# Kernel tuning notes

Measured on AMD Instinct MI355X. Metric: run time of the kernel, lower is better.

The kernel has to match this reference:

```python
import jax, jax.numpy as jnp
import numpy as np
from jax import lax

B, CIN, COUT, K = 4, 128, 128, 3
Z = X = Y = 32
EPS = 1e-8


def setup_inputs() -> dict:
    key = jax.random.key(0)
    k1, k2, k3 = jax.random.split(key, 3)
    x = jax.random.normal(k1, (B, CIN, Z, X, Y), dtype=jnp.float32)
    S = jax.random.normal(k2, (B, CIN), dtype=jnp.float32)
    weight = jax.random.normal(k3, (COUT, CIN, K, K, K), dtype=jnp.float32)
    return {"x": x, "S": S, "weight": weight}


def reference(x, S, weight):
    b, cin, z, xx, yy = x.shape
    cout = weight.shape[0]
    # Per-sample modulated weight: [B, cout, cin, k, k, k]
    W = weight[None] * (S[:, None, :, None, None, None] + 1.0)
    # Demodulation: L2-normalize each (b, cout) filter
    d = lax.rsqrt(jnp.sum(W * W, axis=(2, 3, 4, 5), keepdims=True) + EPS)
    W = W * d
    # Grouped conv3d with groups=B (stride=1, dilation=1 -> same padding = (k-1)//2)
    pad = (K - 1) // 2
    xr = x.reshape(1, b * cin, z, xx, yy)
    Wr = W.reshape(b * cout, cin, K, K, K)
    out = lax.conv_general_dilated(
        xr, Wr,
        window_strides=(1, 1, 1),
        padding=[(pad, pad)] * 3,
        feature_group_count=b,
        dimension_numbers=("NCDHW", "OIDHW", "NCDHW"),
    )
    return out.reshape(b, cout, z, xx, yy)
```

## Files before the change

kernel.cpp:

```cpp
#include <hip/hip_runtime.h>

#define B_    4
#define CIN_  128
#define COUT_ 128
#define EPSF  1e-8f

typedef short  short8  __attribute__((ext_vector_type(8)));
typedef unsigned short ushort8 __attribute__((ext_vector_type(8)));
typedef float  f32x16  __attribute__((ext_vector_type(16)));

__device__ __forceinline__ unsigned short f2bf(float f) {
    union { float f; unsigned int u; } v; v.f = f;
    unsigned int r = (v.u + 0x7fffu + ((v.u >> 16) & 1u)) >> 16;
    return (unsigned short)r;
}

__global__ __launch_bounds__(128) void scale_kernel(const float* __restrict__ S,
                                                    const float* __restrict__ w,
                                                    float* __restrict__ d) {
    const int co = blockIdx.x;
    const int ci = threadIdx.x;
    const float* wp = w + ((size_t)co * CIN_ + ci) * 27;
    float wsq = 0.f;
#pragma unroll
    for (int k = 0; k < 27; ++k) { float v = wp[k]; wsq += v * v; }
    __shared__ float red[128];
    for (int b = 0; b < B_; ++b) {
        float s = S[b * CIN_ + ci] + 1.0f;
        red[ci] = s * s * wsq;
        __syncthreads();
        for (int off = 64; off > 0; off >>= 1) {
            if (ci < off) red[ci] += red[ci + off];
            __syncthreads();
        }
        if (ci == 0) d[b * COUT_ + co] = rsqrtf(red[0] + EPSF);
        __syncthreads();
    }
}

__global__ __launch_bounds__(256) void wt_kernel(const float* __restrict__ w,
                                                 unsigned short* __restrict__ wtf) {
    int idx = blockIdx.x * 256 + threadIdx.x;
    int e  = idx & 7;
    int l  = (idx >> 3) & 63;
    int c  = (idx >> 9) & 7;
    int ct = (idx >> 12) & 3;
    int ko = idx >> 14;
    int co = ct * 32 + (l & 31);
    int ci = c * 16 + (l >> 5) * 8 + e;
    wtf[idx] = f2bf(w[((size_t)co * CIN_ + ci) * 27 + ko]);
}

__global__ __launch_bounds__(256) void xt_kernel(const float* __restrict__ x,
                                                 const float* __restrict__ S,
                                                 unsigned short* __restrict__ xT) {
    __shared__ float ls[128 * 33];
    const int xx = blockIdx.x, z = blockIdx.y, b = blockIdx.z;
    const int tid = threadIdx.x;
    const size_t base = (size_t)b * 4194304 + (size_t)z * 1024 + xx * 32;
#pragma unroll
    for (int it = 0; it < 4; ++it) {
        int i = tid + it * 256;
        int ci = i >> 3, y4 = (i & 7) * 4;
        float4 v = *(const float4*)(x + base + (size_t)ci * 32768 + y4);
        float s = S[b * CIN_ + ci] + 1.0f;
        ls[ci * 33 + y4 + 0] = v.x * s;
        ls[ci * 33 + y4 + 1] = v.y * s;
        ls[ci * 33 + y4 + 2] = v.z * s;
        ls[ci * 33 + y4 + 3] = v.w * s;
    }
    __syncthreads();
    const size_t obase = (size_t)((b * 32 + z) * 32 + xx) * 4096;
#pragma unroll
    for (int it = 0; it < 2; ++it) {
        int i = tid + it * 256;
        int y = i >> 4, c = (i >> 1) & 7, h = i & 1;
        ushort8 v;
#pragma unroll
        for (int j = 0; j < 8; ++j) v[j] = f2bf(ls[(c * 16 + h * 8 + j) * 33 + y]);
        *(ushort8*)(xT + obase + c * 512 + y * 16 + h * 8) = v;
    }
}

__global__ __launch_bounds__(256, 2) void conv_mfma(const unsigned short* __restrict__ xT,
                                                    const unsigned short* __restrict__ wtf,
                                                    const float* __restrict__ dscale,
                                                    float* __restrict__ out) {
    __shared__ char smem[2][26112];
    const int tid  = threadIdx.x;
    const int lane = tid & 63;
    const int wv   = tid >> 6;
    const int z0 = (blockIdx.x >> 4) * 4;
    const int x0 = (blockIdx.x & 15) * 2;
    const int b  = blockIdx.y;

    int goff[7];
    const int lbase = tid * 16;
#pragma unroll
    for (int s = 0; s < 7; ++s) {
        int g = tid + s * 256;
        goff[s] = -2;
        if (g < 1632) {
            int row = g / 68, rem = g - row * 68;
            int h = rem / 34, yi = rem - h * 34;
            int zg = z0 + (row >> 2) - 1;
            int xg = x0 + (row & 3) - 1;
            goff[s] = -1;
            if ((unsigned)zg < 32u && (unsigned)xg < 32u && yi >= 1 && yi <= 32)
                goff[s] = ((b * 32 + zg) * 32 + xg) * 8192 + (yi - 1) * 32 + h * 16;
        }
    }

    const char* xTb = (const char*)xT;
    const char* wtb = (const char*)wtf;
    const int bperlane = ((lane >> 5) * 34 + (lane & 31)) * 16;
    const int aperlane = lane * 16;

    f32x16 acc[4][2];
#pragma unroll
    for (int cz = 0; cz < 4; ++cz)
#pragma unroll
        for (int cx = 0; cx < 2; ++cx)
#pragma unroll
            for (int r = 0; r < 16; ++r) acc[cz][cx][r] = 0.f;

    ushort8 st[7];
#pragma unroll
    for (int s = 0; s < 7; ++s) {
        ushort8 v = {0, 0, 0, 0, 0, 0, 0, 0};
        if (goff[s] >= 0) v = *(const ushort8*)(xTb + goff[s]);
        st[s] = v;
    }
#pragma unroll
    for (int s = 0; s < 7; ++s)
        if (goff[s] != -2) *(ushort8*)(&smem[0][0] + lbase + s * 4096) = st[s];
    __syncthreads();

    for (int c = 0; c < 8; ++c) {
        if (c < 7) {
#pragma unroll
            for (int s = 0; s < 7; ++s) {
                ushort8 v = {0, 0, 0, 0, 0, 0, 0, 0};
                if (goff[s] >= 0) v = *(const ushort8*)(xTb + goff[s] + (c + 1) * 1024);
                st[s] = v;
            }
        }
        const char* buf   = smem[c & 1];
        const char* abase = wtb + c * 1024 + wv * 8192;
#pragma unroll
        for (int ky = 0; ky < 3; ++ky) {
            short8 a[9];
#pragma unroll
            for (int t = 0; t < 9; ++t)
                a[t] = *(const short8*)(abase + (t * 3 + ky) * 32768 + aperlane);
#pragma unroll
            for (int zr = 0; zr < 6; ++zr) {
                short8 bf[4];
#pragma unroll
                for (int xr = 0; xr < 4; ++xr)
                    bf[xr] = *(const short8*)(buf + ((zr * 4 + xr) * 68 + ky) * 16 + bperlane);
#pragma unroll
                for (int cz = 0; cz < 4; ++cz) {
                    const int kz = zr - cz;
                    if (kz >= 0 && kz <= 2) {
#pragma unroll
                        for (int cx = 0; cx < 2; ++cx)
#pragma unroll
                        for (int kx = 0; kx < 3; ++kx)
                            acc[cz][cx] = __builtin_amdgcn_mfma_f32_32x32x16_bf16(
                                a[kz * 3 + kx], bf[cx + kx], acc[cz][cx], 0, 0, 0);
                    }
                }
            }
        }
        if (c < 7) {
            char* nbuf = smem[(c + 1) & 1];
#pragma unroll
            for (int s = 0; s < 7; ++s)
                if (goff[s] != -2) *(ushort8*)(nbuf + lbase + s * 4096) = st[s];
        }
        __syncthreads();
    }

    float dd[16];
#pragma unroll
    for (int r = 0; r < 16; ++r)
        dd[r] = dscale[b * COUT_ + wv * 32 + (r & 3) + 8 * (r >> 2) + 4 * (lane >> 5)];
#pragma unroll
    for (int cz = 0; cz < 4; ++cz)
#pragma unroll
    for (int cx = 0; cx < 2; ++cx) {
        size_t ob = (((size_t)(b * COUT_ + wv * 32) * 32 + (z0 + cz)) * 32 + (x0 + cx)) * 32 + (lane & 31);
#pragma unroll
        for (int r = 0; r < 16; ++r) {
            int row = (r & 3) + 8 * (r >> 2) + 4 * (lane >> 5);
            out[ob + (size_t)row * 32768] = acc[cz][cx][r] * dd[r];
        }
    }
}

__global__ __launch_bounds__(256, 4) void conv_kernel(const float* __restrict__ x,
                                                      const float* __restrict__ S,
                                                      const float* __restrict__ w,
                                                      const float* __restrict__ dscale,
                                                      float* __restrict__ out) {
    __shared__ float xs[6][6][36];
    __shared__ float wsm[27][16];
    const int tid = threadIdx.x;
    const int zt  = blockIdx.x >> 3;
    const int xt  = blockIdx.x & 7;
    const int co0 = blockIdx.y * 16;
    const int b   = blockIdx.z;
    const int z0 = zt * 4, x0 = xt * 4;
    const int lane = tid & 63;
    const int cg = tid >> 6;
    const int zz = (lane >> 4) & 3;
    const int xx = (lane >> 2) & 3;
    const int y0 = (lane & 3) * 8;
    float acc[4][8];
#pragma unroll
    for (int c = 0; c < 4; ++c)
#pragma unroll
        for (int j = 0; j < 8; ++j) acc[c][j] = 0.f;
    for (int ci = 0; ci < CIN_; ++ci) {
        __syncthreads();
        const float* xb = x + (size_t)(b * CIN_ + ci) * 32768;
        const float smod = S[b * CIN_ + ci] + 1.0f;
#pragma unroll
        for (int t = 0; t < 5; ++t) {
            int i = tid + t * 256;
            if (i < 6 * 6 * 34) {
                int zi = i / 204, r = i - zi * 204, xi = r / 34, yi = r - xi * 34;
                int z = z0 + zi - 1, xc = x0 + xi - 1, y = yi - 1;
                float v = 0.f;
                if ((unsigned)z < 32u && (unsigned)xc < 32u && (unsigned)y < 32u)
                    v = xb[z * 1024 + xc * 32 + y] * smod;
                xs[zi][xi][yi] = v;
            }
        }
#pragma unroll
        for (int t = 0; t < 2; ++t) {
            int i = tid + t * 256;
            if (i < 16 * 27) {
                int cog = i / 27, k = i - cog * 27;
                wsm[k][cog] = w[((size_t)(co0 + cog) * CIN_ + ci) * 27 + k];
            }
        }
        __syncthreads();
#pragma unroll
        for (int kz = 0; kz < 3; ++kz)
#pragma unroll
        for (int kx = 0; kx < 3; ++kx) {
            const float* xrow = &xs[zz + kz][xx + kx][y0];
            float xw[10];
#pragma unroll
            for (int q = 0; q < 10; ++q) xw[q] = xrow[q];
            const int kb = (kz * 3 + kx) * 3;
#pragma unroll
            for (int ky = 0; ky < 3; ++ky) {
                float4 wvv = *(const float4*)&wsm[kb + ky][cg * 4];
#pragma unroll
                for (int j = 0; j < 8; ++j) {
                    acc[0][j] = fmaf(xw[ky + j], wvv.x, acc[0][j]);
                    acc[1][j] = fmaf(xw[ky + j], wvv.y, acc[1][j]);
                    acc[2][j] = fmaf(xw[ky + j], wvv.z, acc[2][j]);
                    acc[3][j] = fmaf(xw[ky + j], wvv.w, acc[3][j]);
                }
            }
        }
    }
#pragma unroll
    for (int c = 0; c < 4; ++c) {
        const int co = co0 + cg * 4 + c;
        const float dd = dscale[b * COUT_ + co];
        float* ob = out + (((size_t)(b * COUT_ + co) * 32 + (z0 + zz)) * 32 + (x0 + xx)) * 32 + y0;
#pragma unroll
        for (int j = 0; j < 8; ++j) ob[j] = acc[c][j] * dd;
    }
}

extern "C" void kernel_launch(void* const* d_in, const int* in_sizes, int n_in,
                              void* d_out, int out_size, void* d_ws, size_t ws_size,
                              hipStream_t stream) {
    const float* x = (const float*)d_in[0];
    const float* S = (const float*)d_in[1];
    const float* w = (const float*)d_in[2];
    float* out = (float*)d_out;

    const size_t NEED = 1048576 + 33554432;
    if (ws_size >= NEED) {
        float* dscale = (float*)d_ws;
        unsigned short* wtf = (unsigned short*)((char*)d_ws + 4096);
        unsigned short* xT  = (unsigned short*)((char*)d_ws + 1048576);
        scale_kernel<<<dim3(COUT_), dim3(128), 0, stream>>>(S, w, dscale);
        wt_kernel<<<dim3(1728), dim3(256), 0, stream>>>(w, wtf);
        xt_kernel<<<dim3(32, 32, 4), dim3(256), 0, stream>>>(x, S, xT);
        conv_mfma<<<dim3(128, 4), dim3(256), 0, stream>>>(xT, wtf, dscale, out);
    } else {
        float* dscale = (float*)d_ws;
        scale_kernel<<<dim3(COUT_), dim3(128), 0, stream>>>(S, w, dscale);
        conv_kernel<<<dim3(64, 8, 4), dim3(256), 0, stream>>>(x, S, w, dscale, out);
    }
}
```

Before: 115.5 us.

## Stage input halo via direct global-to-LDS loads and prefetch B fragments

Replaces the register-staged global→LDS copy of the input tile with global_load_lds direct transfers, pointing out-of-bounds halo slots to a zeroed page instead of branching. The B-fragment LDS reads are double-buffered across z rows so the next row loads while MFMAs run, and s_setprio raises wave priority around the MFMA cluster. This frees the staging registers and removes the ds_write step. It adds a memset launch and a zero page in the workspace, and relies on the barrier ordering for the asynchronous LDS writes.

Measured after the change: 121.3 us. 1.05x slower.

```diff
diff --git a/kernel.cpp b/kernel.cpp
--- a/kernel.cpp
+++ b/kernel.cpp
@@ -8,6 +8,10 @@
 typedef short  short8  __attribute__((ext_vector_type(8)));
 typedef unsigned short ushort8 __attribute__((ext_vector_type(8)));
 typedef float  f32x16  __attribute__((ext_vector_type(16)));
+
+#define GLOAD_LDS16(g, l) __builtin_amdgcn_global_load_lds( \
+    (const __attribute__((address_space(1))) unsigned int*)(g), \
+    (__attribute__((address_space(3))) unsigned int*)(l), 16, 0, 0)
 
 __device__ __forceinline__ unsigned short f2bf(float f) {
     union { float f; unsigned int u; } v; v.f = f;
@@ -85,6 +89,7 @@
 __global__ __launch_bounds__(256, 2) void conv_mfma(const unsigned short* __restrict__ xT,
                                                     const unsigned short* __restrict__ wtf,
                                                     const float* __restrict__ dscale,
+                                                    const char* __restrict__ zpage,
                                                     float* __restrict__ out) {
     __shared__ char smem[2][26112];
     const int tid  = threadIdx.x;
@@ -94,27 +99,23 @@
     const int x0 = (blockIdx.x & 15) * 2;
     const int b  = blockIdx.y;
 
-    int goff[7];
-    const int lbase = tid * 16;
+    const char* xTb = (const char*)xT;
+    const char* gsrc[7];
 #pragma unroll
     for (int s = 0; s < 7; ++s) {
         int g = tid + s * 256;
-        goff[s] = -2;
-        if (g < 1632) {
-            int row = g / 68, rem = g - row * 68;
-            int h = rem / 34, yi = rem - h * 34;
-            int zg = z0 + (row >> 2) - 1;
-            int xg = x0 + (row & 3) - 1;
-            goff[s] = -1;
-            if ((unsigned)zg < 32u && (unsigned)xg < 32u && yi >= 1 && yi <= 32)
-                goff[s] = ((b * 32 + zg) * 32 + xg) * 8192 + (yi - 1) * 32 + h * 16;
-        }
-    }
-
-    const char* xTb = (const char*)xT;
-    const char* wtb = (const char*)wtf;
+        int row = g / 68, rem = g - row * 68;
+        int h = rem / 34, yi = rem - h * 34;
+        int zg = z0 + (row >> 2) - 1;
+        int xg = x0 + (row & 3) - 1;
+        bool ok = ((unsigned)zg < 32u) && ((unsigned)xg < 32u) && (yi >= 1) && (yi <= 32);
+        gsrc[s] = ok ? (xTb + ((((b * 32 + zg) * 32 + xg) * 8192) + (yi - 1) * 32 + h * 16))
+                     : zpage;
+    }
+
     const int bperlane = ((lane >> 5) * 34 + (lane & 31)) * 16;
     const int aperlane = lane * 16;
+    const char* wtb = (const char*)wtf;
 
     f32x16 acc[4][2];
 #pragma unroll
@@ -124,26 +125,22 @@
 #pragma unroll
             for (int r = 0; r < 16; ++r) acc[cz][cx][r] = 0.f;
 
-    ushort8 st[7];
-#pragma unroll
-    for (int s = 0; s < 7; ++s) {
-        ushort8 v = {0, 0, 0, 0, 0, 0, 0, 0};
-        if (goff[s] >= 0) v = *(const ushort8*)(xTb + goff[s]);
-        st[s] = v;
-    }
-#pragma unroll
-    for (int s = 0; s < 7; ++s)
-        if (goff[s] != -2) *(ushort8*)(&smem[0][0] + lbase + s * 4096) = st[s];
+#pragma unroll
+    for (int s = 0; s < 6; ++s)
+        GLOAD_LDS16(gsrc[s], &smem[0][tid * 16 + s * 4096]);
+    if (tid < 96)
+        GLOAD_LDS16(gsrc[6], &smem[0][tid * 16 + 6 * 4096]);
     __syncthreads();
 
     for (int c = 0; c < 8; ++c) {
         if (c < 7) {
-#pragma unroll
-            for (int s = 0; s < 7; ++s) {
-                ushort8 v = {0, 0, 0, 0, 0, 0, 0, 0};
-                if (goff[s] >= 0) v = *(const ushort8*)(xTb + goff[s] + (c + 1) * 1024);
-                st[s] = v;
-            }
+            const int nb = (c + 1) & 1;
+            const int coff = (c + 1) * 1024;
+#pragma unroll
+            for (int s = 0; s < 6; ++s)
+                GLOAD_LDS16(gsrc[s] + coff, &smem[nb][tid * 16 + s * 4096]);
+            if (tid < 96)
+                GLOAD_LDS16(gsrc[6] + coff, &smem[nb][tid * 16 + 6 * 4096]);
         }
         const char* buf   = smem[c & 1];
         const char* abase = wtb + c * 1024 + wv * 8192;
@@ -153,12 +150,19 @@
 #pragma unroll
             for (int t = 0; t < 9; ++t)
                 a[t] = *(const short8*)(abase + (t * 3 + ky) * 32768 + aperlane);
+            short8 bf[2][4];
+#pragma unroll
+            for (int xr = 0; xr < 4; ++xr)
+                bf[0][xr] = *(const short8*)(buf + (xr * 68 + ky) * 16 + bperlane);
 #pragma unroll
             for (int zr = 0; zr < 6; ++zr) {
-                short8 bf[4];
-#pragma unroll
-                for (int xr = 0; xr < 4; ++xr)
-                    bf[xr] = *(const short8*)(buf + ((zr * 4 + xr) * 68 + ky) * 16 + bperlane);
+                if (zr < 5) {
+#pragma unroll
+                    for (int xr = 0; xr < 4; ++xr)
+                        bf[(zr + 1) & 1][xr] = *(const short8*)(buf +
+                            (((zr + 1) * 4 + xr) * 68 + ky) * 16 + bperlane);
+                }
+                __builtin_amdgcn_s_setprio(1);
 #pragma unroll
                 for (int cz = 0; cz < 4; ++cz) {
                     const int kz = zr - cz;
@@ -168,16 +172,11 @@
 #pragma unroll
                         for (int kx = 0; kx < 3; ++kx)
                             acc[cz][cx] = __builtin_amdgcn_mfma_f32_32x32x16_bf16(
-                                a[kz * 3 + kx], bf[cx + kx], acc[cz][cx], 0, 0, 0);
+                                a[kz * 3 + kx], bf[zr & 1][cx + kx], acc[cz][cx], 0, 0, 0);
                     }
                 }
+                __builtin_amdgcn_s_setprio(0);
             }
-        }
-        if (c < 7) {
-            char* nbuf = smem[(c + 1) & 1];
-#pragma unroll
-            for (int s = 0; s < 7; ++s)
-                if (goff[s] != -2) *(ushort8*)(nbuf + lbase + s * 4096) = st[s];
         }
         __syncthreads();
     }
@@ -290,12 +289,14 @@
     const size_t NEED = 1048576 + 33554432;
     if (ws_size >= NEED) {
         float* dscale = (float*)d_ws;
-        unsigned short* wtf = (unsigned short*)((char*)d_ws + 4096);
+        char*  zpage  = (char*)d_ws + 4096;
+        unsigned short* wtf = (unsigned short*)((char*)d_ws + 12288);
         unsigned short* xT  = (unsigned short*)((char*)d_ws + 1048576);
+        hipMemsetAsync(zpage, 0, 8192, stream);
         scale_kernel<<<dim3(COUT_), dim3(128), 0, stream>>>(S, w, dscale);
         wt_kernel<<<dim3(1728), dim3(256), 0, stream>>>(w, wtf);
         xt_kernel<<<dim3(32, 32, 4), dim3(256), 0, stream>>>(x, S, xT);
-        conv_mfma<<<dim3(128, 4), dim3(256), 0, stream>>>(xT, wtf, dscale, out);
+        conv_mfma<<<dim3(128, 4), dim3(256), 0, stream>>>(xT, wtf, dscale, zpage, out);
     } else {
         float* dscale = (float*)d_ws;
         scale_kernel<<<dim3(COUT_), dim3(128), 0, stream>>>(S, w, dscale);
```
